# Kernel tuning notes

Measured on AMD Instinct MI355X. Metric: run time of the kernel, lower is better.

## Reference

```python
import jax, jax.numpy as jnp
import numpy as np

ALPHA = 2.0  # spikingjelly ATan default

@jax.custom_vjp
def atan_spike(x):
    # Heaviside forward
    return (x >= 0).astype(x.dtype)

def _atan_fwd(x):
    return atan_spike(x), x

def _atan_bwd(x, g):
    c = (jnp.pi / 2.0) * ALPHA
    return (g * (ALPHA / 2.0) / (1.0 + (c * x) ** 2),)

atan_spike.defvjp(_atan_fwd, _atan_bwd)

def setup_inputs() -> dict:
    key = jax.random.key(0)
    k1, k2 = jax.random.split(key)
    T, B, N = 32, 128, 16384
    x_seq = jax.random.normal(k1, (T, B, N), dtype=jnp.float32)
    beta_raw = jnp.asarray(2.0, dtype=jnp.float32)  # _beta param; beta = sigmoid(_beta)
    return {"x_seq": x_seq, "beta_raw": beta_raw}

def reference(x_seq, beta_raw):
    beta = jax.nn.sigmoid(beta_raw)
    one = jnp.asarray(1.0, x_seq.dtype)

    def step(v, x_t):
        v = beta * v + x_t
        s = atan_spike(v - one)
        # hard reset, detach_reset=True
        v = v * (one - jax.lax.stop_gradient(s))
        return v, s

    v0 = jnp.zeros_like(x_seq[0])
    _, s_seq = jax.lax.scan(step, v0, x_seq)
    return s_seq
```

## Files before the change

kernel.cpp:

```cpp
#include <hip/hip_runtime.h>


#define T_STEPS 32
#define CH 4

typedef float    vfloat4 __attribute__((ext_vector_type(4)));
typedef unsigned vuint4  __attribute__((ext_vector_type(4)));

#define ISSUE(buf, tc)                                                        \
    _Pragma("unroll")                                                         \
    for (int k = 0; k < CH; ++k) {                                            \
        unsigned voff = base16 + (unsigned)((tc) + k) * stride16;             \
        asm volatile("global_load_dwordx4 %0, %1, %2"                         \
                     : "=v"(buf[k])                                           \
                     : "v"(voff), "s"(xp));                                   \
    }

#define WAITN(n) asm volatile("s_waitcnt vmcnt(" #n ")" ::: "memory")

#define FENCE(buf)                                                            \
    _Pragma("unroll")                                                         \
    for (int k = 0; k < CH; ++k) asm volatile("" : "+v"(buf[k]));

#define SCAN(buf, tc)                                                         \
    _Pragma("unroll")                                                         \
    for (int k = 0; k < CH; ++k) {                                            \
        vfloat4 xt = buf[k];                                                  \
        _Pragma("unroll")                                                     \
        for (int c = 0; c < 4; ++c) {                                         \
               \
            v[c] = __fadd_rn(__fmul_rn(beta, v[c]), xt[c]);                   \
                                \
            float d  = __fadd_rn(v[c], -1.0f);                                \
            float sf = (d >= 0.0f) ? 1.0f : 0.0f;                             \
            sp[c] |= ((d >= 0.0f) ? 1u : 0u) << ((tc) + k);                   \
                                     \
            v[c] *= (1.0f - sf);                                              \
        }                                                                     \
    }

__global__ __launch_bounds__(256, 4) void plif_scan_kernel(
    const vfloat4* __restrict__ xp, const float* __restrict__ beta_raw,
    vuint4* __restrict__ bp, int bn4)
{
    int i = blockIdx.x * blockDim.x + threadIdx.x;
    if (i >= bn4) return;

    float beta = 1.0f / (1.0f + expf(-beta_raw[0]));
    asm volatile("" : "+v"(beta));

    unsigned base16   = (unsigned)i * 16u;
    unsigned stride16 = (unsigned)bn4 * 16u;

    vfloat4 v = (vfloat4)(0.0f, 0.0f, 0.0f, 0.0f);
    unsigned sp[4] = {0u, 0u, 0u, 0u};
    vfloat4 A[CH], B[CH];

    ISSUE(A, 0);
    ISSUE(B, 4);
    WAITN(4); FENCE(A); SCAN(A,  0); ISSUE(A,  8);
    WAITN(4); FENCE(B); SCAN(B,  4); ISSUE(B, 12);
    WAITN(4); FENCE(A); SCAN(A,  8); ISSUE(A, 16);
    WAITN(4); FENCE(B); SCAN(B, 12); ISSUE(B, 20);
    WAITN(4); FENCE(A); SCAN(A, 16); ISSUE(A, 24);
    WAITN(4); FENCE(B); SCAN(B, 20); ISSUE(B, 28);
    WAITN(4); FENCE(A); SCAN(A, 24);
    WAITN(0); FENCE(B); SCAN(B, 28);

    vuint4 bits; bits[0]=sp[0]; bits[1]=sp[1]; bits[2]=sp[2]; bits[3]=sp[3];
    bp[i] = bits;
}

__global__ __launch_bounds__(256, 4) void plif_expand_kernel(
    vfloat4* op, int bn4)
{
    int i = blockIdx.x * blockDim.x + threadIdx.x;
    if (i >= bn4) return;

    vuint4 u = *((const vuint4*)op + i);
    asm volatile("" : "+v"(u) :: "memory");

    _Pragma("unroll")
    for (int t = 0; t < T_STEPS; ++t) {
        vfloat4 s;
        _Pragma("unroll")
        for (int c = 0; c < 4; ++c)
            s[c] = ((u[c] >> t) & 1u) ? 1.0f : 0.0f;
        op[i + t * bn4] = s;
    }
}

extern "C" void kernel_launch(void* const* d_in, const int* in_sizes, int n_in,
                              void* d_out, int out_size, void* d_ws, size_t ws_size,
                              hipStream_t stream) {
    const float* x        = (const float*)d_in[0];
    const float* beta_raw = (const float*)d_in[1];
    float* out            = (float*)d_out;

    int total = in_sizes[0];
    int bn    = total / T_STEPS;
    int bn4   = bn / 4;

    dim3 block(256);
    dim3 grid((bn4 + block.x - 1) / block.x);
    plif_scan_kernel<<<grid, block, 0, stream>>>(
        (const vfloat4*)x, beta_raw, (vuint4*)out, bn4);
    plif_expand_kernel<<<grid, block, 0, stream>>>(
        (vfloat4*)out, bn4);
}
```

Measured before the change: 468.8 us.

## Scan bitmask into workspace and expand per timestep with contiguous linear writes

The scan kernel now writes its packed spike bitmask to the workspace instead of the output buffer. A new expand kernel assigns one timestep per grid row, and each block writes a contiguous chunk of output, replacing per-thread strided writes across all timesteps. The intent is more streaming-friendly store patterns. The trade-off is that the bitmask is re-read once per timestep, relying on cache hits. A fallback keeps the old in-place path when the workspace is too small or sizes don't divide.

Result: no change. 469.7 us (+0.2%).

```diff
diff --git a/kernel.cpp b/kernel.cpp
--- a/kernel.cpp
+++ b/kernel.cpp
@@ -3,6 +3,8 @@
 
 #define T_STEPS 32
 #define CH 4
+#define K2_ITERS 32
+#define K2_SLOTS_PER_BLOCK (256 * K2_ITERS)
 
 typedef float    vfloat4 __attribute__((ext_vector_type(4)));
 typedef unsigned vuint4  __attribute__((ext_vector_type(4)));
@@ -71,7 +73,26 @@
     bp[i] = bits;
 }
 
-__global__ __launch_bounds__(256, 4) void plif_expand_kernel(
+__global__ __launch_bounds__(256, 4) void plif_expand_linear(
+    const vuint4* __restrict__ wsbits, vfloat4* __restrict__ op, int bn4)
+{
+    int t = blockIdx.y;
+    unsigned s0 = blockIdx.x * (unsigned)K2_SLOTS_PER_BLOCK + threadIdx.x;
+    const vuint4* wp   = wsbits + s0;
+    vfloat4*      outp = op + (size_t)t * (unsigned)bn4 + s0;
+
+    _Pragma("unroll")
+    for (int k = 0; k < K2_ITERS; ++k) {
+        vuint4 u = wp[k * 256];
+        vfloat4 s;
+        _Pragma("unroll")
+        for (int c = 0; c < 4; ++c)
+            s[c] = ((u[c] >> t) & 1u) ? 1.0f : 0.0f;
+        outp[k * 256] = s;
+    }
+}
+
+__global__ __launch_bounds__(256, 4) void plif_expand_inplace(
     vfloat4* op, int bn4)
 {
     int i = blockIdx.x * blockDim.x + threadIdx.x;
@@ -103,8 +124,20 @@
 
     dim3 block(256);
     dim3 grid((bn4 + block.x - 1) / block.x);
-    plif_scan_kernel<<<grid, block, 0, stream>>>(
-        (const vfloat4*)x, beta_raw, (vuint4*)out, bn4);
-    plif_expand_kernel<<<grid, block, 0, stream>>>(
-        (vfloat4*)out, bn4);
+
+    bool use_ws = (ws_size >= (size_t)bn4 * 16u) &&
+                  (bn4 % K2_SLOTS_PER_BLOCK == 0);
+
+    if (use_ws) {
+        plif_scan_kernel<<<grid, block, 0, stream>>>(
+            (const vfloat4*)x, beta_raw, (vuint4*)d_ws, bn4);
+        dim3 g2(bn4 / K2_SLOTS_PER_BLOCK, T_STEPS);
+        plif_expand_linear<<<g2, block, 0, stream>>>(
+            (const vuint4*)d_ws, (vfloat4*)out, bn4);
+    } else {
+        plif_scan_kernel<<<grid, block, 0, stream>>>(
+            (const vfloat4*)x, beta_raw, (vuint4*)out, bn4);
+        plif_expand_inplace<<<grid, block, 0, stream>>>(
+            (vfloat4*)out, bn4);
+    }
 }
```
